# Kernel optimization log

Hardware: AMD Instinct MI355X
Metric: run time of the kernel (lower is better)

Reference implementation:

```python
import jax, jax.numpy as jnp
from jax import lax
import numpy as np

N_LINKS = 15  # N=30 -> N/2


def _conv1d(x, w, b, pad=0):
    # x: (N,C,L), w: (Cout,Cin,k) torch layout
    y = lax.conv_general_dilated(x, w, (1,), [(pad, pad)],
                                 dimension_numbers=('NCH', 'OIH', 'NCH'))
    return y + b[None, :, None]


def _convT1d(x, w, b, pad=0):
    # torch ConvTranspose1d weight layout: (Cin,Cout,k); stride=1 transpose conv
    # equals conv with flipped kernel and padding k-1-pad
    k = w.shape[-1]
    wc = jnp.flip(w, -1).transpose(1, 0, 2)  # (Cout,Cin,k)
    y = lax.conv_general_dilated(x, wc, (1,), [(k - 1 - pad, k - 1 - pad)],
                                 dimension_numbers=('NCH', 'OIH', 'NCH'))
    return y + b[None, :, None]


def _adaptive_pool_mat(L_in, L_out):
    # PyTorch AdaptiveAvgPool1d: window i = [floor(i*L/out), ceil((i+1)*L/out))
    M = np.zeros((L_out, L_in), dtype=np.float32)
    for i in range(L_out):
        s = (i * L_in) // L_out
        e = -((-(i + 1) * L_in) // L_out)
        M[i, s:e] = 1.0 / (e - s)
    return jnp.asarray(M)

_DS_MAT = _adaptive_pool_mat(13, 5)                       # downsample 13 -> 5
_UP_IDX = np.floor(np.arange(13) * 5 / 13).astype(np.int32)  # nearest 5 -> 13


def setup_inputs() -> dict:
    key = jax.random.key(0)
    ks = jax.random.split(key, 20)
    rn = lambda k, s: jax.random.normal(k, s, jnp.float32) * 0.1
    return {
        'x': jax.random.normal(ks[0], (1, 189), jnp.float32),
        'conv1_w': rn(ks[1], (6, 12, 3)), 'conv1_b': rn(ks[2], (6,)),
        'conv2_w': rn(ks[3], (4, 6, 3)), 'conv2_b': rn(ks[4], (4,)),
        'conv3_w': rn(ks[5], (4, 4, 3)), 'conv3_b': rn(ks[6], (4,)),
        'emb1_w': rn(ks[7], (4, 6, 1)), 'emb1_b': rn(ks[8], (4,)),
        'emb2_w': rn(ks[9], (4, 4, 1)), 'emb2_b': rn(ks[10], (4,)),
        'dec1_w': rn(ks[11], (4, 4, 3)), 'dec1_b': rn(ks[12], (4,)),
        'dec2_w': rn(ks[13], (4, 2, 3)), 'dec2_b': rn(ks[14], (2,)),
        'dec3_w': rn(ks[15], (2, 2, 3)), 'dec3_b': rn(ks[16], (2,)),
        'dec4_w': rn(ks[17], (14, 6, 3)), 'dec4_b': rn(ks[18], (6,)),
    }


def reference(x, conv1_w, conv1_b, conv2_w, conv2_b, conv3_w, conv3_b,
              emb1_w, emb1_b, emb2_w, emb2_b, dec1_w, dec1_b,
              dec2_w, dec2_b, dec3_w, dec3_b, dec4_w, dec4_b):
    afun = jnp.tanh
    obs = x[:, :7]
    obsd = x[:, 95:101]  # 7 + 15*6 - 2 = 95
    # psi = third z-y-z Euler angle of quaternion (w,x,y,z) = obs[0,3:7]
    qw, qx, qy, qz = obs[0, 3], obs[0, 4], obs[0, 5], obs[0, 6]
    psi = jnp.arctan2(qz, qw) - jnp.arctan2(-qx, qy)
    psi = lax.stop_gradient(psi).reshape(1, 1)  # computed via numpy in torch -> detached
    ext_obs = jnp.concatenate([psi, obsd[:, -1:]], axis=1)  # (1,2)
    z2 = jnp.zeros((1, 2), x.dtype)
    jl = jnp.concatenate([z2, x[:, 7:95]], axis=1).reshape(1, 6, N_LINKS)
    jdl = jnp.concatenate([z2, x[:, 101:189]], axis=1).reshape(1, 6, N_LINKS)
    jcat = jnp.concatenate([jl, jdl], axis=1)  # (1,12,15)

    fm_c1 = afun(_conv1d(jcat, conv1_w, conv1_b))            # (1,6,13)
    fm_c1_ds = jnp.einsum('ncl,ol->nco', fm_c1, _DS_MAT)      # (1,6,5)
    fm_c2 = afun(_conv1d(fm_c1_ds, conv2_w, conv2_b))         # (1,4,3)
    fm_c3 = afun(_conv1d(fm_c2, conv3_w, conv3_b))            # (1,4,1)
    fm_links = jnp.mean(fm_c3, axis=2, keepdims=True)         # (1,4,1)

    emb_in = jnp.concatenate([fm_links, ext_obs[:, :, None]], axis=1)  # (1,6,1)
    emb_1 = afun(_conv1d(emb_in, emb1_w, emb1_b))             # (1,4,1)
    emb_2 = afun(_conv1d(emb_1, emb2_w, emb2_b))              # (1,4,1)

    fm_dc1 = afun(_convT1d(emb_2, dec1_w, dec1_b))            # (1,4,3)
    fm_dc2 = afun(_convT1d(fm_dc1, dec2_w, dec2_b))           # (1,2,5)
    fm_dc2_us = fm_dc2[:, :, _UP_IDX]                         # (1,2,13) nearest upsample
    fm_dc3 = afun(_convT1d(fm_dc2_us, dec3_w, dec3_b))        # (1,2,15)
    fm_dc4 = _convT1d(jnp.concatenate([fm_dc3, jcat], axis=1), dec4_w, dec4_b, pad=1)  # (1,6,15)

    acts = fm_dc4.reshape(1, -1)  # (1,90)
    return acts[:, 2:]            # (1,88)
```

## Files before the change

### kernel.cpp

```cpp
#include <hip/hip_runtime.h>
#include <math.h>

__global__ __launch_bounds__(128) void convpolicy_kernel(
    const float* __restrict__ x,
    const float* __restrict__ w1, const float* __restrict__ b1,
    const float* __restrict__ w2, const float* __restrict__ b2,
    const float* __restrict__ w3, const float* __restrict__ b3,
    const float* __restrict__ e1w, const float* __restrict__ e1b,
    const float* __restrict__ e2w, const float* __restrict__ e2b,
    const float* __restrict__ d1w, const float* __restrict__ d1b,
    const float* __restrict__ d2w, const float* __restrict__ d2b,
    const float* __restrict__ d3w, const float* __restrict__ d3b,
    const float* __restrict__ d4w, const float* __restrict__ d4b,
    float* __restrict__ out)
{
    __shared__ float jcat[180];
    __shared__ float fmc1[78];
    __shared__ float dsb[30];
    __shared__ float fmc2[12];
    __shared__ float embin[6];
    __shared__ float emb1[4];
    __shared__ float emb2[4];
    __shared__ float dc1[12];
    __shared__ float dc2[10];
    __shared__ float usb[26];
    __shared__ float dc3[30];
    __shared__ float psi_s;

    const int tid = threadIdx.x;

    for (int idx = tid; idx < 180; idx += 128) {
        float v;
        if (idx < 90) {
            v = (idx < 2) ? 0.f : x[5 + idx];
        } else {
            int f = idx - 90;
            v = (f < 2) ? 0.f : x[99 + f];
        }
        jcat[idx] = v;
    }
    if (tid == 0) {
        float qw = x[3], qx = x[4], qy = x[5], qz = x[6];
        psi_s = atan2f(qz, qw) - atan2f(-qx, qy);
    }
    __syncthreads();

    if (tid < 78) {
        int o = tid / 13, i = tid % 13;
        float acc = b1[o];
        const float* wr = w1 + o * 36;
        #pragma unroll
        for (int c = 0; c < 12; ++c)
            #pragma unroll
            for (int k = 0; k < 3; ++k)
                acc += wr[c * 3 + k] * jcat[c * 15 + i + k];
        fmc1[tid] = tanhf(acc);
    }
    __syncthreads();

    if (tid < 30) {
        int c = tid / 5, o = tid % 5;
        int s = (o * 13) / 5;
        int e = ((o + 1) * 13 + 4) / 5;
        float acc = 0.f;
        for (int l = s; l < e; ++l) acc += fmc1[c * 13 + l];
        dsb[tid] = acc / (float)(e - s);
    }
    __syncthreads();

    if (tid < 12) {
        int o = tid / 3, i = tid % 3;
        float acc = b2[o];
        const float* wr = w2 + o * 18;
        #pragma unroll
        for (int c = 0; c < 6; ++c)
            #pragma unroll
            for (int k = 0; k < 3; ++k)
                acc += wr[c * 3 + k] * dsb[c * 5 + i + k];
        fmc2[tid] = tanhf(acc);
    }
    __syncthreads();

    if (tid < 4) {
        float acc = b3[tid];
        const float* wr = w3 + tid * 12;
        #pragma unroll
        for (int c = 0; c < 4; ++c)
            #pragma unroll
            for (int k = 0; k < 3; ++k)
                acc += wr[c * 3 + k] * fmc2[c * 3 + k];
        embin[tid] = tanhf(acc);
    } else if (tid == 4) {
        embin[4] = psi_s;
    } else if (tid == 5) {
        embin[5] = x[100];
    }
    __syncthreads();

    if (tid < 4) {
        float acc = e1b[tid];
        #pragma unroll
        for (int c = 0; c < 6; ++c) acc += e1w[tid * 6 + c] * embin[c];
        emb1[tid] = tanhf(acc);
    }
    __syncthreads();

    if (tid < 4) {
        float acc = e2b[tid];
        #pragma unroll
        for (int c = 0; c < 4; ++c) acc += e2w[tid * 4 + c] * emb1[c];
        emb2[tid] = tanhf(acc);
    }
    __syncthreads();

    if (tid < 12) {
        int o = tid / 3, t = tid % 3;
        float acc = d1b[o];
        #pragma unroll
        for (int c = 0; c < 4; ++c)
            acc += d1w[c * 12 + o * 3 + t] * emb2[c];
        dc1[tid] = tanhf(acc);
    }
    __syncthreads();

    if (tid < 10) {
        int o = tid / 5, t = tid % 5;
        float acc = d2b[o];
        int ilo = (t - 2 > 0) ? t - 2 : 0;
        int ihi = (t < 2) ? t : 2;
        for (int c = 0; c < 4; ++c)
            for (int i = ilo; i <= ihi; ++i)
                acc += d2w[c * 6 + o * 3 + (t - i)] * dc1[c * 3 + i];
        dc2[tid] = tanhf(acc);
    }
    __syncthreads();

    if (tid < 26) {
        int c = tid / 13, l = tid % 13;
        usb[tid] = dc2[c * 5 + (l * 5) / 13];
    }
    __syncthreads();

    if (tid < 30) {
        int o = tid / 15, t = tid % 15;
        float acc = d3b[o];
        int ilo = (t - 2 > 0) ? t - 2 : 0;
        int ihi = (t < 12) ? t : 12;
        for (int c = 0; c < 2; ++c)
            for (int i = ilo; i <= ihi; ++i)
                acc += d3w[c * 6 + o * 3 + (t - i)] * usb[c * 13 + i];
        dc3[tid] = tanhf(acc);
    }
    __syncthreads();

    if (tid < 88) {
        int g = tid + 2;
        int o = g / 15, t = g % 15;
        float acc = d4b[o];
        int ilo = (t - 1 > 0) ? t - 1 : 0;
        int ihi = (t + 1 < 14) ? t + 1 : 14;
        for (int c = 0; c < 14; ++c) {
            const float* src = (c < 2) ? (dc3 + c * 15) : (jcat + (c - 2) * 15);
            for (int i = ilo; i <= ihi; ++i)
                acc += d4w[c * 18 + o * 3 + (t - i + 1)] * src[i];
        }
        out[tid] = acc;
    }
}

extern "C" void kernel_launch(void* const* d_in, const int* in_sizes, int n_in,
                              void* d_out, int out_size, void* d_ws, size_t ws_size,
                              hipStream_t stream) {
    const float* x   = (const float*)d_in[0];
    const float* w1  = (const float*)d_in[1];
    const float* b1  = (const float*)d_in[2];
    const float* w2  = (const float*)d_in[3];
    const float* b2  = (const float*)d_in[4];
    const float* w3  = (const float*)d_in[5];
    const float* b3  = (const float*)d_in[6];
    const float* e1w = (const float*)d_in[7];
    const float* e1b = (const float*)d_in[8];
    const float* e2w = (const float*)d_in[9];
    const float* e2b = (const float*)d_in[10];
    const float* d1w = (const float*)d_in[11];
    const float* d1b = (const float*)d_in[12];
    const float* d2w = (const float*)d_in[13];
    const float* d2b = (const float*)d_in[14];
    const float* d3w = (const float*)d_in[15];
    const float* d3b = (const float*)d_in[16];
    const float* d4w = (const float*)d_in[17];
    const float* d4b = (const float*)d_in[18];
    float* out = (float*)d_out;

    convpolicy_kernel<<<1, 128, 0, stream>>>(
        x, w1, b1, w2, b2, w3, b3, e1w, e1b, e2w, e2b,
        d1w, d1b, d2w, d2b, d3w, d3b, d4w, d4b, out);
}
```

Baseline: 98.88 us.

## Prefetch all weights into shared memory up front and use fast tanh

All weights and biases are loaded in parallel into one shared buffer at kernel start, using 256 threads. This removes the dependent global-memory loads that previously sat on the serial critical path of each small layer. The x[100] read is also hoisted into the prologue, and tanhf is replaced by an exp/reciprocal approximation with input clamping. This adds a branchy segment-selection prologue and slightly lower tanh accuracy.

```diff
diff --git a/kernel.cpp b/kernel.cpp
--- a/kernel.cpp
+++ b/kernel.cpp
@@ -1,7 +1,14 @@
 #include <hip/hip_runtime.h>
 #include <math.h>
 
-__global__ __launch_bounds__(128) void convpolicy_kernel(
+
+__device__ __forceinline__ float tanh_fast(float v) {
+    v = fminf(15.f, fmaxf(-15.f, v));
+    float e = __expf(2.f * v);
+    return (e - 1.f) * __builtin_amdgcn_rcpf(e + 1.f);
+}
+
+__global__ __launch_bounds__(256) void convpolicy_kernel(
     const float* __restrict__ x,
     const float* __restrict__ w1, const float* __restrict__ b1,
     const float* __restrict__ w2, const float* __restrict__ b2,
@@ -14,6 +21,7 @@
     const float* __restrict__ d4w, const float* __restrict__ d4b,
     float* __restrict__ out)
 {
+    __shared__ float wbuf[748];
     __shared__ float jcat[180];
     __shared__ float fmc1[78];
     __shared__ float dsb[30];
@@ -25,36 +33,63 @@
     __shared__ float dc2[10];
     __shared__ float usb[26];
     __shared__ float dc3[30];
-    __shared__ float psi_s;
+    __shared__ float psi_s, xv100;
 
     const int tid = threadIdx.x;
 
-    for (int idx = tid; idx < 180; idx += 128) {
+    #pragma unroll
+    for (int r = 0; r < 3; ++r) {
+        int g = tid + r * 256;
+        if (g < 748) {
+            const float* p = w1; int o = g;
+            #define SEG_STEP(S, P) if (g >= S) { p = P; o = g - S; }
+            SEG_STEP(216, b1)  SEG_STEP(222, w2)  SEG_STEP(294, b2)
+            SEG_STEP(298, w3)  SEG_STEP(346, b3)  SEG_STEP(350, e1w)
+            SEG_STEP(374, e1b) SEG_STEP(378, e2w) SEG_STEP(394, e2b)
+            SEG_STEP(398, d1w) SEG_STEP(446, d1b) SEG_STEP(450, d2w)
+            SEG_STEP(474, d2b) SEG_STEP(476, d3w) SEG_STEP(488, d3b)
+            SEG_STEP(490, d4w) SEG_STEP(742, d4b)
+            #undef SEG_STEP
+            wbuf[g] = p[o];
+        }
+    }
+    if (tid < 180) {
         float v;
-        if (idx < 90) {
-            v = (idx < 2) ? 0.f : x[5 + idx];
+        if (tid < 90) {
+            v = (tid < 2) ? 0.f : x[5 + tid];
         } else {
-            int f = idx - 90;
+            int f = tid - 90;
             v = (f < 2) ? 0.f : x[99 + f];
         }
-        jcat[idx] = v;
-    }
-    if (tid == 0) {
+        jcat[tid] = v;
+    } else if (tid == 180) {
         float qw = x[3], qx = x[4], qy = x[5], qz = x[6];
         psi_s = atan2f(qz, qw) - atan2f(-qx, qy);
-    }
-    __syncthreads();
+    } else if (tid == 181) {
+        xv100 = x[100];
+    }
+    __syncthreads();
+
+    const float* W1  = wbuf;       const float* B1  = wbuf + 216;
+    const float* W2  = wbuf + 222; const float* B2  = wbuf + 294;
+    const float* W3  = wbuf + 298; const float* B3  = wbuf + 346;
+    const float* E1W = wbuf + 350; const float* E1B = wbuf + 374;
+    const float* E2W = wbuf + 378; const float* E2B = wbuf + 394;
+    const float* D1W = wbuf + 398; const float* D1B = wbuf + 446;
+    const float* D2W = wbuf + 450; const float* D2B = wbuf + 474;
+    const float* D3W = wbuf + 476; const float* D3B = wbuf + 488;
+    const float* D4W = wbuf + 490; const float* D4B = wbuf + 742;
 
     if (tid < 78) {
         int o = tid / 13, i = tid % 13;
-        float acc = b1[o];
-        const float* wr = w1 + o * 36;
+        float acc = B1[o];
+        const float* wr = W1 + o * 36;
         #pragma unroll
         for (int c = 0; c < 12; ++c)
             #pragma unroll
             for (int k = 0; k < 3; ++k)
                 acc += wr[c * 3 + k] * jcat[c * 15 + i + k];
-        fmc1[tid] = tanhf(acc);
+        fmc1[tid] = tanh_fast(acc);
     }
     __syncthreads();
 
@@ -70,68 +105,68 @@
 
     if (tid < 12) {
         int o = tid / 3, i = tid % 3;
-        float acc = b2[o];
-        const float* wr = w2 + o * 18;
+        float acc = B2[o];
+        const float* wr = W2 + o * 18;
         #pragma unroll
         for (int c = 0; c < 6; ++c)
             #pragma unroll
             for (int k = 0; k < 3; ++k)
                 acc += wr[c * 3 + k] * dsb[c * 5 + i + k];
-        fmc2[tid] = tanhf(acc);
+        fmc2[tid] = tanh_fast(acc);
     }
     __syncthreads();
 
     if (tid < 4) {
-        float acc = b3[tid];
-        const float* wr = w3 + tid * 12;
+        float acc = B3[tid];
+        const float* wr = W3 + tid * 12;
         #pragma unroll
         for (int c = 0; c < 4; ++c)
             #pragma unroll
             for (int k = 0; k < 3; ++k)
                 acc += wr[c * 3 + k] * fmc2[c * 3 + k];
-        embin[tid] = tanhf(acc);
+        embin[tid] = tanh_fast(acc);
     } else if (tid == 4) {
         embin[4] = psi_s;
     } else if (tid == 5) {
-        embin[5] = x[100];
+        embin[5] = xv100;
     }
     __syncthreads();
 
     if (tid < 4) {
-        float acc = e1b[tid];
-        #pragma unroll
-        for (int c = 0; c < 6; ++c) acc += e1w[tid * 6 + c] * embin[c];
-        emb1[tid] = tanhf(acc);
+        float acc = E1B[tid];
+        #pragma unroll
+        for (int c = 0; c < 6; ++c) acc += E1W[tid * 6 + c] * embin[c];
+        emb1[tid] = tanh_fast(acc);
     }
     __syncthreads();
 
     if (tid < 4) {
-        float acc = e2b[tid];
-        #pragma unroll
-        for (int c = 0; c < 4; ++c) acc += e2w[tid * 4 + c] * emb1[c];
-        emb2[tid] = tanhf(acc);
+        float acc = E2B[tid];
+        #pragma unroll
+        for (int c = 0; c < 4; ++c) acc += E2W[tid * 4 + c] * emb1[c];
+        emb2[tid] = tanh_fast(acc);
     }
     __syncthreads();
 
     if (tid < 12) {
         int o = tid / 3, t = tid % 3;
-        float acc = d1b[o];
+        float acc = D1B[o];
         #pragma unroll
         for (int c = 0; c < 4; ++c)
-            acc += d1w[c * 12 + o * 3 + t] * emb2[c];
-        dc1[tid] = tanhf(acc);
+            acc += D1W[c * 12 + o * 3 + t] * emb2[c];
+        dc1[tid] = tanh_fast(acc);
     }
     __syncthreads();
 
     if (tid < 10) {
         int o = tid / 5, t = tid % 5;
-        float acc = d2b[o];
+        float acc = D2B[o];
         int ilo = (t - 2 > 0) ? t - 2 : 0;
         int ihi = (t < 2) ? t : 2;
         for (int c = 0; c < 4; ++c)
             for (int i = ilo; i <= ihi; ++i)
-                acc += d2w[c * 6 + o * 3 + (t - i)] * dc1[c * 3 + i];
-        dc2[tid] = tanhf(acc);
+                acc += D2W[c * 6 + o * 3 + (t - i)] * dc1[c * 3 + i];
+        dc2[tid] = tanh_fast(acc);
     }
     __syncthreads();
 
@@ -143,26 +178,26 @@
 
     if (tid < 30) {
         int o = tid / 15, t = tid % 15;
-        float acc = d3b[o];
+        float acc = D3B[o];
         int ilo = (t - 2 > 0) ? t - 2 : 0;
         int ihi = (t < 12) ? t : 12;
         for (int c = 0; c < 2; ++c)
             for (int i = ilo; i <= ihi; ++i)
-                acc += d3w[c * 6 + o * 3 + (t - i)] * usb[c * 13 + i];
-        dc3[tid] = tanhf(acc);
+                acc += D3W[c * 6 + o * 3 + (t - i)] * usb[c * 13 + i];
+        dc3[tid] = tanh_fast(acc);
     }
     __syncthreads();
 
     if (tid < 88) {
         int g = tid + 2;
         int o = g / 15, t = g % 15;
-        float acc = d4b[o];
+        float acc = D4B[o];
         int ilo = (t - 1 > 0) ? t - 1 : 0;
         int ihi = (t + 1 < 14) ? t + 1 : 14;
         for (int c = 0; c < 14; ++c) {
             const float* src = (c < 2) ? (dc3 + c * 15) : (jcat + (c - 2) * 15);
             for (int i = ilo; i <= ihi; ++i)
-                acc += d4w[c * 18 + o * 3 + (t - i + 1)] * src[i];
+                acc += D4W[c * 18 + o * 3 + (t - i + 1)] * src[i];
         }
         out[tid] = acc;
     }
@@ -192,7 +227,7 @@
     const float* d4b = (const float*)d_in[18];
     float* out = (float*)d_out;
 
-    convpolicy_kernel<<<1, 128, 0, stream>>>(
+    convpolicy_kernel<<<1, 256, 0, stream>>>(
         x, w1, b1, w2, b2, w3, b3, e1w, e1b, e2w, e2b,
         d1w, d1b, d2w, d2b, d3w, d3b, d4w, d4b, out);
 }
```

Measured after the change: 94.20 us. -4.7%, faster.

## Preload all weights into LDS with float4 loads, single wavefront, fast tanh

Applied to the files above, without the earlier changes.

All weights, biases and the input vector are bulk-loaded into shared memory up front with vectorized float4 loads, so the serial chain of tiny layers reads LDS instead of issuing dependent global loads at each stage. The block shrinks to one 64-lane wavefront, with loops covering the wider stages, which makes barriers cheaper. tanhf is replaced by an exp/reciprocal approximation, and the two atan2 calls run on separate lanes. The risks are small accuracy differences from the fast tanh, and longer serial stages for conv1 and dec4 with only 64 threads.

```diff
diff --git a/kernel.cpp b/kernel.cpp
--- a/kernel.cpp
+++ b/kernel.cpp
@@ -1,7 +1,32 @@
 #include <hip/hip_runtime.h>
 #include <math.h>
 
-__global__ __launch_bounds__(128) void convpolicy_kernel(
+__device__ __forceinline__ float tanh_fast(float v) {
+    v = fminf(15.f, fmaxf(-15.f, v));
+    float e = __expf(2.f * v);
+    return (e - 1.f) * __builtin_amdgcn_rcpf(e + 1.f);
+}
+
+#define O_W1  0
+#define O_B1  216
+#define O_W2  224
+#define O_B2  296
+#define O_W3  300
+#define O_B3  348
+#define O_E1W 352
+#define O_E1B 376
+#define O_E2W 380
+#define O_E2B 396
+#define O_D1W 400
+#define O_D1B 448
+#define O_D2W 452
+#define O_D2B 476
+#define O_D3W 480
+#define O_D3B 492
+#define O_D4W 496
+#define O_D4B 748
+
+__global__ __launch_bounds__(64) void convpolicy_kernel(
     const float* __restrict__ x,
     const float* __restrict__ w1, const float* __restrict__ b1,
     const float* __restrict__ w2, const float* __restrict__ b2,
@@ -14,157 +39,190 @@
     const float* __restrict__ d4w, const float* __restrict__ d4b,
     float* __restrict__ out)
 {
+    __shared__ __align__(16) float wbuf[756];
+    __shared__ __align__(16) float xbuf[192];
     __shared__ float jcat[180];
     __shared__ float fmc1[78];
     __shared__ float dsb[30];
     __shared__ float fmc2[12];
     __shared__ float embin[6];
-    __shared__ float emb1[4];
-    __shared__ float emb2[4];
+    __shared__ float emb1v[4];
+    __shared__ float emb2v[4];
     __shared__ float dc1[12];
     __shared__ float dc2[10];
     __shared__ float usb[26];
     __shared__ float dc3[30];
-    __shared__ float psi_s;
-
-    const int tid = threadIdx.x;
-
-    for (int idx = tid; idx < 180; idx += 128) {
-        float v;
-        if (idx < 90) {
-            v = (idx < 2) ? 0.f : x[5 + idx];
-        } else {
-            int f = idx - 90;
-            v = (f < 2) ? 0.f : x[99 + f];
+    __shared__ float at2[2];
+
+    const int l = threadIdx.x;
+
+    if (l < 54) *(float4*)(wbuf + O_W1  + 4 * l) = ((const float4*)w1)[l];
+    if (l < 63) *(float4*)(wbuf + O_D4W + 4 * l) = ((const float4*)d4w)[l];
+    if (l < 18)      *(float4*)(wbuf + O_W2  + 4 * l)        = ((const float4*)w2)[l];
+    else if (l < 30) *(float4*)(wbuf + O_W3  + 4 * (l - 18)) = ((const float4*)w3)[l - 18];
+    else if (l < 42) *(float4*)(wbuf + O_D1W + 4 * (l - 30)) = ((const float4*)d1w)[l - 30];
+    else if (l < 48) *(float4*)(wbuf + O_E1W + 4 * (l - 42)) = ((const float4*)e1w)[l - 42];
+    else if (l < 54) *(float4*)(wbuf + O_D2W + 4 * (l - 48)) = ((const float4*)d2w)[l - 48];
+    else if (l < 58) *(float4*)(wbuf + O_E2W + 4 * (l - 54)) = ((const float4*)e2w)[l - 54];
+    else if (l < 61) *(float4*)(wbuf + O_D3W + 4 * (l - 58)) = ((const float4*)d3w)[l - 58];
+    if (l < 6)       wbuf[O_B1  + l]      = b1[l];
+    else if (l < 10) wbuf[O_B2  + l - 6]  = b2[l - 6];
+    else if (l < 14) wbuf[O_B3  + l - 10] = b3[l - 10];
+    else if (l < 18) wbuf[O_E1B + l - 14] = e1b[l - 14];
+    else if (l < 22) wbuf[O_E2B + l - 18] = e2b[l - 18];
+    else if (l < 26) wbuf[O_D1B + l - 22] = d1b[l - 22];
+    else if (l < 28) wbuf[O_D2B + l - 26] = d2b[l - 26];
+    else if (l < 30) wbuf[O_D3B + l - 28] = d3b[l - 28];
+    else if (l < 36) wbuf[O_D4B + l - 30] = d4b[l - 30];
+    if (l < 47)      *(float4*)(xbuf + 4 * l) = ((const float4*)x)[l];
+    else if (l == 47) xbuf[188] = x[188];
+    __syncthreads();
+
+    if (l < 2) {
+        float yy = (l == 0) ? xbuf[6] : -xbuf[4];
+        float xx = (l == 0) ? xbuf[3] : xbuf[5];
+        at2[l] = atan2f(yy, xx);
+    }
+    #pragma unroll
+    for (int r = 0; r < 3; ++r) {
+        int g = l + 64 * r;
+        if (g < 180) {
+            float v;
+            if (g < 90) v = (g < 2) ? 0.f : xbuf[5 + g];
+            else { int f = g - 90; v = (f < 2) ? 0.f : xbuf[99 + f]; }
+            jcat[g] = v;
         }
-        jcat[idx] = v;
-    }
-    if (tid == 0) {
-        float qw = x[3], qx = x[4], qy = x[5], qz = x[6];
-        psi_s = atan2f(qz, qw) - atan2f(-qx, qy);
-    }
-    __syncthreads();
-
-    if (tid < 78) {
-        int o = tid / 13, i = tid % 13;
-        float acc = b1[o];
-        const float* wr = w1 + o * 36;
-        #pragma unroll
-        for (int c = 0; c < 12; ++c)
+    }
+    __syncthreads();
+
+    #pragma unroll
+    for (int r = 0; r < 2; ++r) {
+        int g = l + 64 * r;
+        if (g < 78) {
+            int o = g / 13, i = g % 13;
+            float acc = wbuf[O_B1 + o];
+            const float* wr = wbuf + O_W1 + o * 36;
             #pragma unroll
-            for (int k = 0; k < 3; ++k)
-                acc += wr[c * 3 + k] * jcat[c * 15 + i + k];
-        fmc1[tid] = tanhf(acc);
-    }
-    __syncthreads();
-
-    if (tid < 30) {
-        int c = tid / 5, o = tid % 5;
+            for (int c = 0; c < 12; ++c)
+                #pragma unroll
+                for (int k = 0; k < 3; ++k)
+                    acc += wr[c * 3 + k] * jcat[c * 15 + i + k];
+            fmc1[g] = tanh_fast(acc);
+        }
+    }
+    __syncthreads();
+
+    if (l < 30) {
+        int c = l / 5, o = l % 5;
         int s = (o * 13) / 5;
         int e = ((o + 1) * 13 + 4) / 5;
         float acc = 0.f;
-        for (int l = s; l < e; ++l) acc += fmc1[c * 13 + l];
-        dsb[tid] = acc / (float)(e - s);
-    }
-    __syncthreads();
-
-    if (tid < 12) {
-        int o = tid / 3, i = tid % 3;
-        float acc = b2[o];
-        const float* wr = w2 + o * 18;
+        for (int i = s; i < e; ++i) acc += fmc1[c * 13 + i];
+        dsb[l] = acc / (float)(e - s);
+    }
+    __syncthreads();
+
+    if (l < 12) {
+        int o = l / 3, i = l % 3;
+        float acc = wbuf[O_B2 + o];
+        const float* wr = wbuf + O_W2 + o * 18;
         #pragma unroll
         for (int c = 0; c < 6; ++c)
             #pragma unroll
             for (int k = 0; k < 3; ++k)
                 acc += wr[c * 3 + k] * dsb[c * 5 + i + k];
-        fmc2[tid] = tanhf(acc);
-    }
-    __syncthreads();
-
-    if (tid < 4) {
-        float acc = b3[tid];
-        const float* wr = w3 + tid * 12;
+        fmc2[l] = tanh_fast(acc);
+    }
+    __syncthreads();
+
+    if (l < 4) {
+        float acc = wbuf[O_B3 + l];
+        const float* wr = wbuf + O_W3 + l * 12;
         #pragma unroll
         for (int c = 0; c < 4; ++c)
             #pragma unroll
             for (int k = 0; k < 3; ++k)
                 acc += wr[c * 3 + k] * fmc2[c * 3 + k];
-        embin[tid] = tanhf(acc);
-    } else if (tid == 4) {
-        embin[4] = psi_s;
-    } else if (tid == 5) {
-        embin[5] = x[100];
-    }
-    __syncthreads();
-
-    if (tid < 4) {
-        float acc = e1b[tid];
-        #pragma unroll
-        for (int c = 0; c < 6; ++c) acc += e1w[tid * 6 + c] * embin[c];
-        emb1[tid] = tanhf(acc);
-    }
-    __syncthreads();
-
-    if (tid < 4) {
-        float acc = e2b[tid];
-        #pragma unroll
-        for (int c = 0; c < 4; ++c) acc += e2w[tid * 4 + c] * emb1[c];
-        emb2[tid] = tanhf(acc);
-    }
-    __syncthreads();
-
-    if (tid < 12) {
-        int o = tid / 3, t = tid % 3;
-        float acc = d1b[o];
+        embin[l] = tanh_fast(acc);
+    } else if (l == 4) {
+        embin[4] = at2[0] - at2[1];
+    } else if (l == 5) {
+        embin[5] = xbuf[100];
+    }
+    __syncthreads();
+
+    if (l < 4) {
+        float acc = wbuf[O_E1B + l];
+        #pragma unroll
+        for (int c = 0; c < 6; ++c) acc += wbuf[O_E1W + l * 6 + c] * embin[c];
+        emb1v[l] = tanh_fast(acc);
+    }
+    __syncthreads();
+
+    if (l < 4) {
+        float acc = wbuf[O_E2B + l];
+        #pragma unroll
+        for (int c = 0; c < 4; ++c) acc += wbuf[O_E2W + l * 4 + c] * emb1v[c];
+        emb2v[l] = tanh_fast(acc);
+    }
+    __syncthreads();
+
+    if (l < 12) {
+        int o = l / 3, t = l % 3;
+        float acc = wbuf[O_D1B + o];
         #pragma unroll
         for (int c = 0; c < 4; ++c)
-            acc += d1w[c * 12 + o * 3 + t] * emb2[c];
-        dc1[tid] = tanhf(acc);
-    }
-    __syncthreads();
-
-    if (tid < 10) {
-        int o = tid / 5, t = tid % 5;
-        float acc = d2b[o];
+            acc += wbuf[O_D1W + c * 12 + o * 3 + t] * emb2v[c];
+        dc1[l] = tanh_fast(acc);
+    }
+    __syncthreads();
+
+    if (l < 10) {
+        int o = l / 5, t = l % 5;
+        float acc = wbuf[O_D2B + o];
         int ilo = (t - 2 > 0) ? t - 2 : 0;
         int ihi = (t < 2) ? t : 2;
         for (int c = 0; c < 4; ++c)
             for (int i = ilo; i <= ihi; ++i)
-                acc += d2w[c * 6 + o * 3 + (t - i)] * dc1[c * 3 + i];
-        dc2[tid] = tanhf(acc);
-    }
-    __syncthreads();
-
-    if (tid < 26) {
-        int c = tid / 13, l = tid % 13;
-        usb[tid] = dc2[c * 5 + (l * 5) / 13];
-    }
-    __syncthreads();
-
-    if (tid < 30) {
-        int o = tid / 15, t = tid % 15;
-        float acc = d3b[o];
+                acc += wbuf[O_D2W + c * 6 + o * 3 + (t - i)] * dc1[c * 3 + i];
+        dc2[l] = tanh_fast(acc);
+    }
+    __syncthreads();
+
+    if (l < 26) {
+        int c = l / 13, i = l % 13;
+        usb[l] = dc2[c * 5 + (i * 5) / 13];
+    }
+    __syncthreads();
+
+    if (l < 30) {
+        int o = l / 15, t = l % 15;
+        float acc = wbuf[O_D3B + o];
         int ilo = (t - 2 > 0) ? t - 2 : 0;
         int ihi = (t < 12) ? t : 12;
         for (int c = 0; c < 2; ++c)
             for (int i = ilo; i <= ihi; ++i)
-                acc += d3w[c * 6 + o * 3 + (t - i)] * usb[c * 13 + i];
-        dc3[tid] = tanhf(acc);
-    }
-    __syncthreads();
-
-    if (tid < 88) {
-        int g = tid + 2;
-        int o = g / 15, t = g % 15;
-        float acc = d4b[o];
-        int ilo = (t - 1 > 0) ? t - 1 : 0;
-        int ihi = (t + 1 < 14) ? t + 1 : 14;
-        for (int c = 0; c < 14; ++c) {
-            const float* src = (c < 2) ? (dc3 + c * 15) : (jcat + (c - 2) * 15);
-            for (int i = ilo; i <= ihi; ++i)
-                acc += d4w[c * 18 + o * 3 + (t - i + 1)] * src[i];
+                acc += wbuf[O_D3W + c * 6 + o * 3 + (t - i)] * usb[c * 13 + i];
+        dc3[l] = tanh_fast(acc);
+    }
+    __syncthreads();
+
+    #pragma unroll
+    for (int r = 0; r < 2; ++r) {
+        int idx = l + 64 * r;
+        if (idx < 88) {
+            int g = idx + 2;
+            int o = g / 15, t = g % 15;
+            float acc = wbuf[O_D4B + o];
+            int ilo = (t - 1 > 0) ? t - 1 : 0;
+            int ihi = (t + 1 < 14) ? t + 1 : 14;
+            for (int c = 0; c < 14; ++c) {
+                const float* src = (c < 2) ? (dc3 + c * 15) : (jcat + (c - 2) * 15);
+                for (int i = ilo; i <= ihi; ++i)
+                    acc += wbuf[O_D4W + c * 18 + o * 3 + (t - i + 1)] * src[i];
+            }
+            out[idx] = acc;
         }
-        out[tid] = acc;
     }
 }
 
@@ -192,7 +250,7 @@
     const float* d4b = (const float*)d_in[18];
     float* out = (float*)d_out;
 
-    convpolicy_kernel<<<1, 128, 0, stream>>>(
+    convpolicy_kernel<<<1, 64, 0, stream>>>(
         x, w1, b1, w2, b2, w3, b3, e1w, e1b, e2w, e2b,
         d1w, d1b, d2w, d2b, d3w, d3b, d4w, d4b, out);
 }
```

New measurement: 103.4 us. 1.05x slower.
